# Kernel optimization log

Measured on AMD Instinct MI355X. Metric: run time of the kernel, lower is better.

Reference implementation:

```python
import jax, jax.numpy as jnp
import numpy as np

N = 50000   # nodes
E = 800000  # edges (avg degree 16)
DIMS = [(128, 128), (128, 128), (128, 64)]  # (in, out) per SAGEConv layer
EPS_BN = 1e-5
EPS_NORM = 1e-12


def _make_layer(key, din, dout):
    k1, k2 = jax.random.split(key)
    s = 1.0 / np.sqrt(din)
    return (
        jax.random.normal(k1, (dout, din), jnp.float32) * s,  # Wl: neighbor linear
        jnp.zeros((dout,), jnp.float32),                      # bl
        jax.random.normal(k2, (dout, din), jnp.float32) * s,  # Wr: root linear (no bias in PyG)
        jnp.ones((dout,), jnp.float32),                       # bn gamma
        jnp.zeros((dout,), jnp.float32),                      # bn beta
        jnp.zeros((dout,), jnp.float32),                      # bn running mean
        jnp.ones((dout,), jnp.float32),                       # bn running var
    )


def setup_inputs() -> dict:
    key = jax.random.key(0)
    kx, ke, k0, k1, k2 = jax.random.split(key, 5)
    inp = {
        "x": jax.random.normal(kx, (N, 128), jnp.float32),
        "edge_index": jax.random.randint(ke, (2, E), 0, N, dtype=jnp.int32),
    }
    for i, (k, (din, dout)) in enumerate(zip([k0, k1, k2], DIMS)):
        Wl, bl, Wr, g, b, rm, rv = _make_layer(k, din, dout)
        inp.update({f"Wl{i}": Wl, f"bl{i}": bl, f"Wr{i}": Wr,
                    f"g{i}": g, f"b{i}": b, f"rm{i}": rm, f"rv{i}": rv})
    return inp


def _sage_conv(x, src, dst, Wl, bl, Wr):
    # mean aggregation of incoming messages: gather src features, scatter-add at dst
    agg = jax.ops.segment_sum(x[src], dst, num_segments=N)          # [N, din]
    deg = jax.ops.segment_sum(jnp.ones((src.shape[0],), x.dtype), dst, num_segments=N)
    mean = agg / jnp.maximum(deg, 1.0)[:, None]
    return mean @ Wl.T + bl + x @ Wr.T


def _bn_eval(x, g, b, rm, rv):
    return g * (x - rm) * jax.lax.rsqrt(rv + EPS_BN) + b


def reference(x, edge_index,
              Wl0, bl0, Wr0, g0, b0, rm0, rv0,
              Wl1, bl1, Wr1, g1, b1, rm1, rv1,
              Wl2, bl2, Wr2, g2, b2, rm2, rv2):
    src, dst = edge_index[0], edge_index[1]
    layers = [
        (Wl0, bl0, Wr0, g0, b0, rm0, rv0),
        (Wl1, bl1, Wr1, g1, b1, rm1, rv1),
        (Wl2, bl2, Wr2, g2, b2, rm2, rv2),
    ]
    h = x
    for i, (Wl, bl, Wr, g, b, rm, rv) in enumerate(layers):
        h = _bn_eval(_sage_conv(h, src, dst, Wl, bl, Wr), g, b, rm, rv)
        if i < len(layers) - 1:
            h = jax.nn.relu(h)  # dropout is identity in eval mode
    # F.normalize(p=2, dim=1)
    return h / jnp.maximum(jnp.linalg.norm(h, axis=1, keepdims=True), EPS_NORM)
```

## Files before the change

kernel.cpp:

```cpp
#include <hip/hip_runtime.h>
#include <hip/hip_bf16.h>

#define CDIV(a,b) (((a)+(b)-1)/(b))
#define NBUCK_MAX 512
#define FUSE_CAP 1536
#define CAPL     4096
#define AGGF_CAP 2048

typedef __attribute__((ext_vector_type(8))) short short8;
typedef __attribute__((ext_vector_type(4))) float f32x4;
typedef __attribute__((ext_vector_type(2))) float f32x2;

static __device__ __forceinline__ unsigned short f2bf(float f){
  union { float f; unsigned u; } v; v.f = f;
  unsigned r = v.u + 0x7fffu + ((v.u >> 16) & 1u);
  return (unsigned short)(r >> 16);
}
static __device__ __forceinline__ unsigned pack2(float lo, float hi){
  return (unsigned)f2bf(lo) | ((unsigned)f2bf(hi) << 16);
}
static __device__ __forceinline__ float bf2f(unsigned short s){
  union { unsigned u; float f; } v; v.u = ((unsigned)s) << 16; return v.f;
}
static __device__ __forceinline__ unsigned pk_fp8x4(float a, float b, float c, float d){
// ... 31 lines not shown
      int kc = a.perm ? (((k & 7) << 4) | (k >> 3)) : k;
      v = a.W0[nn*128 + kc];
    } else {
      v = a.W1[nn*128 + (k - 128)];
    }
    a.Bpk[idx] = f2bf(v);
  } else if (a.do_bn && idx < NB16 + a.dout){
    int jj = idx - NB16;
    float s = a.g[jj] * rsqrtf(a.rv[jj] + 1e-5f);
    a.sc[jj] = s;
    a.sh[jj] = (a.bl[jj] - a.rm[jj]) * s + a.b[jj];
  }
}


__global__ __launch_bounds__(256) void k_prep(const float* __restrict__ x, int n4, unsigned* __restrict__ xb,
                                              unsigned* __restrict__ xq,
                                              const int* __restrict__ dst, int E,
                                              int* __restrict__ bcnt, int nbuck,
                                              int castBlocks, int histBlocks,
                                              WtpArgs a0, WtpArgs a1, WtpArgs a2, WtpArgs a3){
  __shared__ int s[NBUCK_MAX];
  int b = blockIdx.x, t = threadIdx.x;
  if (b < castBlocks){
    int i = b*256 + t;
    if (i < n4){
      float4 v = ((const float4*)x)[i];
      uint2 o; o.x = pack2(v.x, v.y); o.y = pack2(v.z, v.w);
      ((uint2*)xb)[i] = o;
      xq[i] = pk_fp8x4(v.x, v.y, v.z, v.w);
    }
    return;
  }
  b -= castBlocks;
  if (b < histBlocks){
    for (int i=t;i<nbuck;i+=256) s[i] = 0;
    __syncthreads();
    constexpr int EPT = 16;
    int e0 = b*256*EPT;
    #pragma unroll
    for (int i=0;i<EPT;i++){
      int e = e0 + i*256 + t;
      if (e < E) atomicAdd(&s[dst[e] >> 7], 1);
    }
    __syncthreads();
    for (int i=t;i<nbuck;i+=256){
      int c = s[i];
      if (c > 0) atomicAdd(&bcnt[i], c);
    }
    return;
  }
  b -= histBlocks;
  if (b < a0.nblk){ wtp_one(a0, b*256 + t); return; }
  b -= a0.nblk;
  if (b < a1.nblk){ wtp_one(a1, b*256 + t); return; }
  b -= a1.nblk;
  if (b < a2.nblk){ wtp_one(a2, b*256 + t); return; }
  b -= a2.nblk;
  wtp_one(a3, b*256 + t);
}

__global__ __launch_bounds__(256) void k_bucketA(const int* __restrict__ src, const int* __restrict__ dst,
                                                 int E, const int* __restrict__ bcnt,
                                                 int* __restrict__ bcur, unsigned* __restrict__ ebuf, int nbuck){
  __shared__ int scnt[NBUCK_MAX];
  __shared__ int sbase[NBUCK_MAX];
  __shared__ int sboff[NBUCK_MAX];
  __shared__ int ss[256];
  int t = threadIdx.x;
  {
    int a0 = (2*t   < nbuck) ? bcnt[2*t]   : 0;
    int a1 = (2*t+1 < nbuck) ? bcnt[2*t+1] : 0;
    ss[t] = a0 + a1; __syncthreads();
    for (int d=1; d<256; d<<=1){
      int u = (t>=d) ? ss[t-d] : 0;
      __syncthreads();
      ss[t] += u;
      __syncthreads();
    }
    int excl = ss[t] - (a0 + a1);
    if (2*t   < nbuck) sboff[2*t]   = excl;
    if (2*t+1 < nbuck) sboff[2*t+1] = excl + a0;
  }
  for (int i=t;i<nbuck;i+=256) scnt[i] = 0;
  __syncthreads();
  constexpr int EPT = 16;
  int e0 = blockIdx.x*256*EPT;
  int b[EPT]; unsigned pk[EPT];
  #pragma unroll
  for (int i=0;i<EPT;i++){
    int e = e0 + i*256 + t;
    if (e < E){
      int d = dst[e];
      b[i] = d >> 7;
      pk[i] = ((unsigned)(d & 127) << 16) | (unsigned)src[e];
      atomicAdd(&scnt[b[i]], 1);
    } else b[i] = -1;
  }
  __syncthreads();
  for (int i=t;i<nbuck;i+=256){
    int c = scnt[i];
    sbase[i] = (c > 0) ? atomicAdd(&bcur[i], c) : 0;
    scnt[i] = 0;
  }
  __syncthreads();
  #pragma unroll
  for (int i=0;i<EPT;i++){
    if (b[i] >= 0){
      int p = atomicAdd(&scnt[b[i]], 1);
      ebuf[(size_t)sboff[b[i]] + sbase[b[i]] + p] = pk[i];
    }
  }
}


__global__ __launch_bounds__(256, 3) void k_bfuse(
    const unsigned* __restrict__ ebuf, const int* __restrict__ bcnt, int nbuck, int E, int N,
    int* __restrict__ off, int* __restrict__ csr,
    const uint4* __restrict__ xq4, const unsigned short* __restrict__ Ag,
    const unsigned short* __restrict__ Bpk, const float* __restrict__ sc, const float* __restrict__ sh,
    unsigned short* __restrict__ outh, unsigned* __restrict__ outq){
  __shared__ uint4 Ms4[64*17];
  __shared__ int scsr[FUSE_CAP];
  __shared__ int sEx[NBUCK_MAX];
  __shared__ int ss[256];
  unsigned short* Ms = (unsigned short*)Ms4;
  int* sdeg = (int*)Ms4;
  int* sabs = sdeg + 128;
  int* cur  = sabs + 129;
  int bb_ = blockIdx.x;
  int b = bb_ >> 1, hi = bb_ & 1;
  int t = threadIdx.x;
  {
    int a0 = (2*t   < nbuck) ? bcnt[2*t]   : 0;
    int a1 = (2*t+1 < nbuck) ? bcnt[2*t+1] : 0;
    ss[t] = a0 + a1; __syncthreads();
    for (int d=1; d<256; d<<=1){
      int u = (t>=d) ? ss[t-d] : 0;
      __syncthreads();
      ss[t] += u;
      __syncthreads();
    }
    int excl = ss[t] - (a0 + a1);
    if (2*t   < nbuck) sEx[2*t]   = excl;
    if (2*t+1 < nbuck) sEx[2*t+1] = excl + a0;
  }
  if (t < 128){ sdeg[t] = 0; cur[t] = 0; }
  __syncthreads();
  int e0 = sEx[b];
  int e1 = (b+1 < nbuck) ? sEx[b+1] : E;
  for (int e = e0 + t; e < e1; e += 256)
    atomicAdd(&sdeg[ebuf[e] >> 16], 1);
  __syncthreads();
  for (int d=1; d<128; d<<=1){
    int u = (t < 128 && t >= d) ? sdeg[t-d] : 0;
    __syncthreads();
    if (t < 128) sdeg[t] += u;
    __syncthreads();
  }
  if (t == 0) sabs[0] = 0;
  if (t < 128) sabs[t+1] = sdeg[t];
  __syncthreads();
  int base64 = sabs[hi*64];
  int myTot  = sabs[hi*64 + 64] - base64;
  int n0 = (b << 7) + hi*64;
  int cnt = (N > n0) ? min(64, N - n0) : 0;
  if (cnt > 0 && t <= cnt) off[n0 + t] = e0 + sabs[hi*64 + t];
  int lane = t & 63, w = t >> 6, sl = lane & 7;
  int gs0[2], gs1[2];
  #pragma unroll
  for (int it=0; it<2; it++){
    int rk = w*16 + it*8 + (lane >> 3);
    gs0[it] = sabs[hi*64 + rk] - base64;
    gs1[it] = sabs[hi*64 + rk + 1] - base64;
  }
  bool fits = myTot <= FUSE_CAP;
  for (int e = e0 + t; e < e1; e += 256){
    unsigned pr = ebuf[e];
    int ln = (int)(pr >> 16);
    if ((ln >> 6) == hi){
      int p = atomicAdd(&cur[ln], 1);
      int gpos = sabs[ln] + p;
      int sv = (int)(pr & 0xffffu);
      if (fits) scsr[gpos - base64] = sv;
      else      csr[e0 + gpos] = sv;
    }
  }
  __syncthreads();
  const int* gcsr = csr + e0 + base64;
  if (fits){
    for (int i = t; i < myTot; i += 256) csr[e0 + base64 + i] = scsr[i];
  } else {
    for (int i = t; i < FUSE_CAP; i += 256) scsr[i] = gcsr[i];
    __syncthreads();
  }

  #pragma unroll
  for (int it=0; it<2; it++){
    int rk = w*16 + it*8 + (lane >> 3);
    int s0 = gs0[it], s1 = gs1[it];
    f32x2 b0={0,0},b1={0,0},b2={0,0},b3={0,0},b4={0,0},b5={0,0},b6={0,0},b7={0,0};
    int e = s0;
    for (; e + 8 <= s1; e += 8){
      int i0,i1,i2,i3,i4,i5,i6,i7;
      if (e + 8 <= FUSE_CAP){
        i0 = scsr[e];   i1 = scsr[e+1]; i2 = scsr[e+2]; i3 = scsr[e+3];
        i4 = scsr[e+4]; i5 = scsr[e+5]; i6 = scsr[e+6]; i7 = scsr[e+7];
      } else {
        i0 = gcsr[e];   i1 = gcsr[e+1]; i2 = gcsr[e+2]; i3 = gcsr[e+3];
        i4 = gcsr[e+4]; i5 = gcsr[e+5]; i6 = gcsr[e+6]; i7 = gcsr[e+7];
      }
// ... 29 lines not shown
    int d = s1 - s0;
    float inv = 1.0f / (float)(d > 0 ? d : 1);
    uint4 o0, o1;
    o0.x = pack2(b0.x*inv, b0.y*inv);  o0.y = pack2(b1.x*inv, b1.y*inv);
    o0.z = pack2(b2.x*inv, b2.y*inv);  o0.w = pack2(b3.x*inv, b3.y*inv);
    o1.x = pack2(b4.x*inv, b4.y*inv);  o1.y = pack2(b5.x*inv, b5.y*inv);
    o1.z = pack2(b6.x*inv, b6.y*inv);  o1.w = pack2(b7.x*inv, b7.y*inv);
    Ms4[rk*17 + sl*2]     = o0;
    Ms4[rk*17 + sl*2 + 1] = o1;
  }
  __syncthreads();

  int quad = lane >> 4, c = lane & 15;
  int woff = w*16;
  int r0 = n0 + woff + c;

  f32x4 acc[8];
  #pragma unroll
  for (int nt=0;nt<8;nt++) acc[nt] = (f32x4){0.f,0.f,0.f,0.f};

  #pragma unroll
  for (int kk=0; kk<8; kk++){
    int ka = (kk & 3)*32 + quad*8;
    short8 a0;
    if (kk < 4){
      a0 = *(const short8*)&Ms[(woff + c)*136 + ka];
    } else {
      a0 = (short8){0,0,0,0,0,0,0,0};
      if (r0 < N) a0 = *(const short8*)(Ag + (size_t)r0*128 + ka);
    }
    #pragma unroll
    for (int nt=0; nt<8; nt++){
      short8 bb2 = *(const short8*)(Bpk + (size_t)((kk*8 + nt)*64 + lane)*8);
      acc[nt] = __builtin_amdgcn_mfma_f32_16x16x32_bf16(a0, bb2, acc[nt], 0, 0, 0);
    }
  }

  float scv[8], shv[8];
  #pragma unroll
  for (int nt=0;nt<8;nt++){ scv[nt] = sc[nt*16 + c]; shv[nt] = sh[nt*16 + c]; }

  #pragma unroll
  for (int r=0;r<4;r++){
    int row = n0 + woff + quad*4 + r;
    if (row < N){
      float u[8];
      #pragma unroll
      for (int nt=0;nt<8;nt++){
        float uu = acc[nt][r]*scv[nt] + shv[nt];
        u[nt] = fmaxf(uu, 0.f);
        outh[(size_t)row*128 + nt*16 + c] = f2bf(u[nt]);
      }
      uint2 q;
      q.x = pk_fp8x4(u[0], u[1], u[2], u[3]);
      q.y = pk_fp8x4(u[4], u[5], u[6], u[7]);
      ((uint2*)outq)[(size_t)row*16 + c] = q;
    }
  }
}


__global__ __launch_bounds__(256, 3) void k_fuse1(
    const uint4* __restrict__ hq4, const int* __restrict__ off, const int* __restrict__ csr,
    const unsigned short* __restrict__ Ag, const unsigned short* __restrict__ Bpk,
    const float* __restrict__ sc, const float* __restrict__ sh,
    const unsigned short* __restrict__ BpkL,
    unsigned short* __restrict__ outh, unsigned* __restrict__ outyl, int n){
  __shared__ uint4 Ms4[64*17];
  __shared__ uint4 sBL4[1024];
  __shared__ int sw[2];
  unsigned short* Ms = (unsigned short*)Ms4;
  int* scsr = (int*)sBL4;
  int t = threadIdx.x;
  int n0 = blockIdx.x*64;
  if (t < 2) sw[t] = off[min(n0 + t*64, n)];
  __syncthreads();
  int e0b = sw[0];
  int span = sw[1] - e0b;
  for (int i = t; i < span && i < CAPL; i += 256) scsr[i] = csr[e0b + i];
  __syncthreads();

  int lane = t & 63, w = t >> 6;
  int sl = lane & 7;

  #pragma unroll
  for (int it=0; it<2; it++){
    int rk = w*16 + it*8 + (lane >> 3);
    int idx = n0 + rk;
    bool valid = idx < n;
    int s0 = valid ? off[idx]   : 0;
    int s1 = valid ? off[idx+1] : 0;
    f32x2 b0={0,0},b1={0,0},b2={0,0},b3={0,0},b4={0,0},b5={0,0},b6={0,0},b7={0,0};
    int e = s0;
    for (; e + 8 <= s1; e += 8){
      int le = e - e0b;
      int i0,i1,i2,i3,i4,i5,i6,i7;
      if (le + 8 <= CAPL){
        i0 = scsr[le];   i1 = scsr[le+1]; i2 = scsr[le+2]; i3 = scsr[le+3];
        i4 = scsr[le+4]; i5 = scsr[le+5]; i6 = scsr[le+6]; i7 = scsr[le+7];
      } else {
        i0 = csr[e];   i1 = csr[e+1]; i2 = csr[e+2]; i3 = csr[e+3];
        i4 = csr[e+4]; i5 = csr[e+5]; i6 = csr[e+6]; i7 = csr[e+7];
      }
      uint4 v0 = hq4[(size_t)i0*8 + sl];
      uint4 v1 = hq4[(size_t)i1*8 + sl];
      uint4 v2 = hq4[(size_t)i2*8 + sl];
      uint4 v3 = hq4[(size_t)i3*8 + sl];
      uint4 v4 = hq4[(size_t)i4*8 + sl];
      uint4 v5 = hq4[(size_t)i5*8 + sl];
      uint4 v6 = hq4[(size_t)i6*8 + sl];
      uint4 v7 = hq4[(size_t)i7*8 + sl];
      ACCP16(v0); ACCP16(v1); ACCP16(v2); ACCP16(v3);
      ACCP16(v4); ACCP16(v5); ACCP16(v6); ACCP16(v7);
    }
    for (; e + 4 <= s1; e += 4){
      int le = e - e0b;
      int i0,i1,i2,i3;
      if (le + 4 <= CAPL){
        i0 = scsr[le]; i1 = scsr[le+1]; i2 = scsr[le+2]; i3 = scsr[le+3];
      } else {
        i0 = csr[e]; i1 = csr[e+1]; i2 = csr[e+2]; i3 = csr[e+3];
      }
      uint4 v0 = hq4[(size_t)i0*8 + sl];
      uint4 v1 = hq4[(size_t)i1*8 + sl];
      uint4 v2 = hq4[(size_t)i2*8 + sl];
      uint4 v3 = hq4[(size_t)i3*8 + sl];
      ACCP16(v0); ACCP16(v1); ACCP16(v2); ACCP16(v3);
    }
    for (; e < s1; e++){
      int le = e - e0b;
      int ii = (le < CAPL) ? scsr[le] : csr[e];
      uint4 v = hq4[(size_t)ii*8 + sl];
      ACCP16(v);
    }
    int d = s1 - s0;
    float inv = 1.0f / (float)(d > 0 ? d : 1);
    uint4 o0, o1;
    o0.x = pack2(b0.x*inv, b0.y*inv);  o0.y = pack2(b1.x*inv, b1.y*inv);
    o0.z = pack2(b2.x*inv, b2.y*inv);  o0.w = pack2(b3.x*inv, b3.y*inv);
    o1.x = pack2(b4.x*inv, b4.y*inv);  o1.y = pack2(b5.x*inv, b5.y*inv);
    o1.z = pack2(b6.x*inv, b6.y*inv);  o1.w = pack2(b7.x*inv, b7.y*inv);
    Ms4[rk*17 + sl*2]     = o0;
    Ms4[rk*17 + sl*2 + 1] = o1;
  }
  __syncthreads();

  int quad = lane >> 4, c = lane & 15;
  int woff = w*16;
  int r0 = n0 + woff + c;

  f32x4 acc[8];
  #pragma unroll
  for (int nt=0;nt<8;nt++) acc[nt] = (f32x4){0.f,0.f,0.f,0.f};

  #pragma unroll
  for (int kk=0; kk<8; kk++){
    int ka = (kk & 3)*32 + quad*8;
    short8 a0;
    if (kk < 4){
      a0 = *(const short8*)&Ms[(woff + c)*136 + ka];
    } else {
      a0 = (short8){0,0,0,0,0,0,0,0};
      if (r0 < n) a0 = *(const short8*)(Ag + (size_t)r0*128 + ka);
    }
    #pragma unroll
    for (int nt=0; nt<8; nt++){
      short8 bb2 = *(const short8*)(Bpk + (size_t)((kk*8 + nt)*64 + lane)*8);
      acc[nt] = __builtin_amdgcn_mfma_f32_16x16x32_bf16(a0, bb2, acc[nt], 0, 0, 0);
    }
  }

  float scv[8], shv[8];
  #pragma unroll
  for (int nt=0;nt<8;nt++){ scv[nt] = sc[nt*16 + c]; shv[nt] = sh[nt*16 + c]; }

  __syncthreads();

  #pragma unroll
  for (int r=0;r<4;r++){
    int lrow = woff + quad*4 + r;
    int row = n0 + lrow;
    if (row < n){
      float u[8];
      #pragma unroll
      for (int nt=0;nt<8;nt++){
        float uu = acc[nt][r]*scv[nt] + shv[nt];
        u[nt] = fmaxf(uu, 0.f);
        outh[(size_t)row*128 + nt*16 + c] = f2bf(u[nt]);
      }
      #pragma unroll
      for (int nt=0;nt<8;nt++) Ms[lrow*136 + nt*16 + c] = f2bf(u[nt]);
    } else {
      #pragma unroll
      for (int nt=0;nt<8;nt++) Ms[lrow*136 + nt*16 + c] = 0;
    }
  }

  {
    const uint4* sL = (const uint4*)BpkL;
    #pragma unroll
    for (int i=0;i<4;i++) sBL4[i*256 + t] = sL[i*256 + t];
  }
  __syncthreads();
  unsigned short* BsL = (unsigned short*)sBL4;
  f32x4 acc2[4];
  #pragma unroll
  for (int nt=0;nt<4;nt++) acc2[nt] = (f32x4){0.f,0.f,0.f,0.f};
  int r0l = woff + c;
  #pragma unroll
  for (int kk=0; kk<4; kk++){
    int ka = kk*32 + quad*8;
    short8 a0 = *(const short8*)&Ms[r0l*136 + ka];
    #pragma unroll
    for (int nt=0; nt<4; nt++){
      short8 bb2 = *(const short8*)&BsL[(size_t)((kk*4 + nt)*64 + lane)*8];
      acc2[nt] = __builtin_amdgcn_mfma_f32_16x16x32_bf16(a0, bb2, acc2[nt], 0, 0, 0);
    }
  }
  #pragma unroll
  for (int r=0;r<4;r++){
    int row = n0 + woff + quad*4 + r;
    if (row < n){
      unsigned q = pk_fp8x4(acc2[0][r], acc2[1][r], acc2[2][r], acc2[3][r]);
      outyl[(size_t)row*16 + c] = q;
    }
  }
}


__global__ __launch_bounds__(256, 3) void k_aggf(
    const uint4* __restrict__ ylq4, const int* __restrict__ off, const int* __restrict__ csr,
    const unsigned short* __restrict__ A0, const unsigned short* __restrict__ BpkR,
    const float* __restrict__ sc, const float* __restrict__ sh,
    float* __restrict__ outf, int n){
  __shared__ unsigned short Ms[64*64];
  __shared__ unsigned short Bs[128*64];
  __shared__ int scsr[AGGF_CAP];
  __shared__ int sw[2];
  int t = threadIdx.x;
  int n0 = blockIdx.x*64;
  if (t < 2) sw[t] = off[min(n0 + t*64, n)];
  {
    const uint4* s = (const uint4*)BpkR;
    uint4* d = (uint4*)Bs;
    #pragma unroll
    for (int i=0;i<4;i++) d[i*256 + t] = s[i*256 + t];
  }
  __syncthreads();
  int e0b = sw[0];
  int span = sw[1] - e0b;
  for (int i = t; i < span && i < AGGF_CAP; i += 256) scsr[i] = csr[e0b + i];
  __syncthreads();

  int lane = t & 63, w = t >> 6;
  int sl4 = lane & 3;

  {
    int rk = w*16 + (lane >> 2);
    int idx = n0 + rk;
    bool valid = idx < n;
    int s0 = valid ? off[idx]   : 0;
    int s1 = valid ? off[idx+1] : 0;
    f32x2 b0={0,0},b1={0,0},b2={0,0},b3={0,0},b4={0,0},b5={0,0},b6={0,0},b7={0,0};
    int e = s0;
    for (; e + 8 <= s1; e += 8){
      int le = e - e0b;
      int i0,i1,i2,i3,i4,i5,i6,i7;
      if (le + 8 <= AGGF_CAP){
        i0 = scsr[le];   i1 = scsr[le+1]; i2 = scsr[le+2]; i3 = scsr[le+3];
        i4 = scsr[le+4]; i5 = scsr[le+5]; i6 = scsr[le+6]; i7 = scsr[le+7];
      } else {
        i0 = csr[e];   i1 = csr[e+1]; i2 = csr[e+2]; i3 = csr[e+3];
        i4 = csr[e+4]; i5 = csr[e+5]; i6 = csr[e+6]; i7 = csr[e+7];
      }
      uint4 v0 = ylq4[(size_t)i0*4 + sl4];
      uint4 v1 = ylq4[(size_t)i1*4 + sl4];
      uint4 v2 = ylq4[(size_t)i2*4 + sl4];
      uint4 v3 = ylq4[(size_t)i3*4 + sl4];
      uint4 v4 = ylq4[(size_t)i4*4 + sl4];
      uint4 v5 = ylq4[(size_t)i5*4 + sl4];
      uint4 v6 = ylq4[(size_t)i6*4 + sl4];
      uint4 v7 = ylq4[(size_t)i7*4 + sl4];
      ACCP16(v0); ACCP16(v1); ACCP16(v2); ACCP16(v3);
      ACCP16(v4); ACCP16(v5); ACCP16(v6); ACCP16(v7);
    }
    for (; e + 4 <= s1; e += 4){
      int le = e - e0b;
      int i0,i1,i2,i3;
      if (le + 4 <= AGGF_CAP){
        i0 = scsr[le]; i1 = scsr[le+1]; i2 = scsr[le+2]; i3 = scsr[le+3];
      } else {
        i0 = csr[e]; i1 = csr[e+1]; i2 = csr[e+2]; i3 = csr[e+3];
      }
      uint4 v0 = ylq4[(size_t)i0*4 + sl4];
      uint4 v1 = ylq4[(size_t)i1*4 + sl4];
      uint4 v2 = ylq4[(size_t)i2*4 + sl4];
      uint4 v3 = ylq4[(size_t)i3*4 + sl4];
      ACCP16(v0); ACCP16(v1); ACCP16(v2); ACCP16(v3);
    }
    for (; e < s1; e++){
      int le = e - e0b;
      int ii = (le < AGGF_CAP) ? scsr[le] : csr[e];
      uint4 v = ylq4[(size_t)ii*4 + sl4];
      ACCP16(v);
    }
    int d = s1 - s0;
    float inv = 1.0f / (float)(d > 0 ? d : 1);
    uint4 o0, o1;
    o0.x = pack2(b0.x*inv, b0.y*inv);  o0.y = pack2(b1.x*inv, b1.y*inv);
    o0.z = pack2(b2.x*inv, b2.y*inv);  o0.w = pack2(b3.x*inv, b3.y*inv);
    o1.x = pack2(b4.x*inv, b4.y*inv);  o1.y = pack2(b5.x*inv, b5.y*inv);
    o1.z = pack2(b6.x*inv, b6.y*inv);  o1.w = pack2(b7.x*inv, b7.y*inv);
    ((uint4*)Ms)[rk*8 + sl4*2]     = o0;
    ((uint4*)Ms)[rk*8 + sl4*2 + 1] = o1;
  }
  __syncthreads();

  int quad = lane >> 4, c = lane & 15;
  int woff = w*16;
  int r0 = n0 + woff + c;
  f32x4 acc[4];
  #pragma unroll
  for (int nt=0;nt<4;nt++) acc[nt] = (f32x4){0.f,0.f,0.f,0.f};
  #pragma unroll
  for (int kk=0; kk<4; kk++){
    int ka = kk*32 + quad*8;
    short8 a0 = {0,0,0,0,0,0,0,0};
    if (r0 < n) a0 = *(const short8*)(A0 + (size_t)r0*128 + ka);
    #pragma unroll
    for (int nt=0; nt<4; nt++){
      short8 bb2 = *(const short8*)&Bs[(size_t)((kk*4 + nt)*64 + lane)*8];
      acc[nt] = __builtin_amdgcn_mfma_f32_16x16x32_bf16(a0, bb2, acc[nt], 0, 0, 0);
    }
  }

  float scv[4], shv[4];
  #pragma unroll
  for (int nt=0;nt<4;nt++){ scv[nt] = sc[nt*16 + c]; shv[nt] = sh[nt*16 + c]; }

  #pragma unroll
  for (int r=0;r<4;r++){
    int lr = woff + quad*4 + r;
    int row = n0 + lr;
    float v[4];
    float ss2 = 0.f;
    if (row < n){
      #pragma unroll
      for (int nt=0;nt<4;nt++){
        float u = acc[nt][r] + bf2f(Ms[lr*64 + c*4 + nt]);
        u = u*scv[nt] + shv[nt];
        v[nt] = u;
        ss2 += u*u;
      }
    } else {
      #pragma unroll
      for (int nt=0;nt<4;nt++) v[nt] = 0.f;
    }
    ss2 += __shfl_xor(ss2, 1, 64);
    ss2 += __shfl_xor(ss2, 2, 64);
    ss2 += __shfl_xor(ss2, 4, 64);
    ss2 += __shfl_xor(ss2, 8, 64);
    float rn = 1.0f / fmaxf(sqrtf(ss2), 1e-12f);
    if (row < n){
      #pragma unroll
      for (int nt=0;nt<4;nt++) outf[(size_t)row*64 + nt*16 + c] = v[nt]*rn;
    }
  }
}


extern "C" void kernel_launch(void* const* d_in, const int* in_sizes, int n_in,
                              void* d_out, int out_size, void* d_ws, size_t ws_size,
                              hipStream_t stream){
  const float* x = (const float*)d_in[0];
  const int* ei  = (const int*)d_in[1];
  int N = in_sizes[0] / 128;
  int E = in_sizes[1] / 2;
  const int* esrc = ei;
  const int* edst = ei + E;
  int nbuck = CDIV(N, 128);
  int nb2 = 2*nbuck;

  const float *Wl[3], *bl[3], *Wr[3], *g[3], *bb[3], *rm[3], *rv[3];
  int dout[3];
  for (int i=0;i<3;i++){
    int base = 2 + 7*i;
    Wl[i]=(const float*)d_in[base];   bl[i]=(const float*)d_in[base+1];
    Wr[i]=(const float*)d_in[base+2]; g[i] =(const float*)d_in[base+3];
    bb[i]=(const float*)d_in[base+4]; rm[i]=(const float*)d_in[base+5];
    rv[i]=(const float*)d_in[base+6];
    dout[i] = in_sizes[base] / 128;
  }

  char* p = (char*)d_ws;
  size_t o = 0;
  auto alloc = [&](size_t bytes)->void*{ void* r = p + o; o += (bytes + 255) & ~(size_t)255; return r; };
  int* bz    = (int*)alloc((size_t)2*nbuck*4);
  int* bcnt  = bz;
  int* bcur  = bz + nbuck;
  int* off   = (int*)alloc((size_t)(N+1)*4);
  int* csr   = (int*)alloc((size_t)E*4);
  unsigned* ebuf = (unsigned*)alloc((size_t)E*4);
  unsigned* xb   = (unsigned*)alloc((size_t)N*64*4);
  unsigned* xq   = (unsigned*)alloc((size_t)N*128);
  unsigned* h_a  = (unsigned*)alloc((size_t)N*64*4);
  unsigned* haq  = (unsigned*)alloc((size_t)N*128);
  unsigned* h_b  = (unsigned*)alloc((size_t)N*64*4);
  unsigned* ylb  = (unsigned*)alloc((size_t)N*64);
  unsigned short* Bpk01[2];
  float* sc[3]; float* sh[3];
  for (int i=0;i<2;i++) Bpk01[i] = (unsigned short*)alloc((size_t)256*dout[i]*2);
  unsigned short* BpkL = (unsigned short*)alloc((size_t)128*dout[2]*2);
  unsigned short* BpkR = (unsigned short*)alloc((size_t)128*dout[2]*2);
  for (int i=0;i<3;i++){
    sc[i] = (float*)alloc((size_t)dout[i]*4);
    sh[i] = (float*)alloc((size_t)dout[i]*4);
  }

  hipMemsetAsync(bz, 0, (size_t)2*nbuck*4, stream);

  WtpArgs wa[4];
  wa[0] = { Wl[0], Wr[0], bl[0], g[0], bb[0], rm[0], rv[0], Bpk01[0], sc[0], sh[0], 8, dout[0], 1, CDIV(256*dout[0]+dout[0],256), 0 };
  wa[1] = { Wl[1], Wr[1], bl[1], g[1], bb[1], rm[1], rv[1], Bpk01[1], sc[1], sh[1], 8, dout[1], 1, CDIV(256*dout[1]+dout[1],256), 1 };
  wa[2] = { Wl[2], nullptr, nullptr, nullptr, nullptr, nullptr, nullptr, BpkL, nullptr, nullptr, 4, dout[2], 0, CDIV(128*dout[2],256), 0 };
  wa[3] = { Wr[2], nullptr, bl[2], g[2], bb[2], rm[2], rv[2], BpkR, sc[2], sh[2], 4, dout[2], 1, CDIV(128*dout[2]+dout[2],256), 0 };

  int castBlocks = CDIV(N*32, 256);
  int histBlocks = CDIV(E, 256*16);
  int prepBlocks = castBlocks + histBlocks + wa[0].nblk + wa[1].nblk + wa[2].nblk + wa[3].nblk;
  k_prep   <<<prepBlocks,256,0,stream>>>(x, N*32, xb, xq, edst, E, bcnt, nbuck, castBlocks, histBlocks,
                                         wa[0], wa[1], wa[2], wa[3]);
  k_bucketA<<<CDIV(E,256*16),256,0,stream>>>(esrc, edst, E, bcnt, bcur, ebuf, nbuck);

  k_bfuse<<<nb2,256,0,stream>>>(ebuf, bcnt, nbuck, E, N, off, csr,
                                (const uint4*)xq, (const unsigned short*)xb,
                                Bpk01[0], sc[0], sh[0],
                                (unsigned short*)h_a, haq);
  k_fuse1<<<nb2,256,0,stream>>>((const uint4*)haq, off, csr,
                                (const unsigned short*)h_a, Bpk01[1], sc[1], sh[1], BpkL,
                                (unsigned short*)h_b, ylb, N);
  k_aggf<<<nb2,256,0,stream>>>((const uint4*)ylb, off, csr,
                               (const unsigned short*)h_b, BpkR, sc[2], sh[2],
                               (float*)d_out, N);
}
```

Measured before the change: 226.0 us.

## Merge five pipeline kernels into one persistent kernel with grid barriers

Replaces the five separate launches (prep, bucket, bfuse, fuse1, aggf) with a single persistent kernel sized to occupancy. The phases are separated by a software global barrier built on atomic counters, and each phase's work blocks run through grid-stride loops over a shared LDS pool. The bucket phase also halves its edges per block. This is meant to remove launch gaps and tail idle time between kernels. In exchange it adds barrier spin cost, caps occupancy at 2 blocks per CU, and depends on every block being co-resident.

After: 659.2 us. +191.7%, slower.

```diff
diff --git a/kernel.cpp b/kernel.cpp
--- a/kernel.cpp
+++ b/kernel.cpp
@@ -69,63 +69,96 @@
 }
 
 
-__global__ __launch_bounds__(256) void k_prep(const float* __restrict__ x, int n4, unsigned* __restrict__ xb,
-                                              unsigned* __restrict__ xq,
-                                              const int* __restrict__ dst, int E,
-                                              int* __restrict__ bcnt, int nbuck,
-                                              int castBlocks, int histBlocks,
-                                              WtpArgs a0, WtpArgs a1, WtpArgs a2, WtpArgs a3){
-  __shared__ int s[NBUCK_MAX];
-  int b = blockIdx.x, t = threadIdx.x;
-  if (b < castBlocks){
+struct MegaArgs {
+  const float* x; int n4;
+  unsigned* xb; unsigned* xq;
+  const int* esrc; const int* edst;
+  int E, N, nbuck;
+  int* bcnt; int* bcur;
+  int* barCnt; int* barEpoch;
+  int* off; int* csr; unsigned* ebuf;
+  const unsigned short* Bpk0; const unsigned short* Bpk1;
+  const unsigned short* BpkL; const unsigned short* BpkR;
+  const float *sc0, *sh0, *sc1, *sh1, *sc2, *sh2;
+  unsigned short* h_a; unsigned short* h_b;
+  unsigned* haq; unsigned* ylb;
+  float* outf;
+  int castBlocks, histBlocks, p0Total, aBlocks, nb2, nblk;
+  WtpArgs wa0, wa1, wa2, wa3;
+};
+
+static __device__ __forceinline__ void gbar(int* cnt, int* epoch, int nblk, int eps){
+  __syncthreads();
+  if (threadIdx.x == 0){
+    __threadfence();
+    int prev = __hip_atomic_fetch_add(cnt, 1, __ATOMIC_ACQ_REL, __HIP_MEMORY_SCOPE_AGENT);
+    if (prev == nblk - 1){
+      __hip_atomic_store(cnt, 0, __ATOMIC_RELAXED, __HIP_MEMORY_SCOPE_AGENT);
+      __hip_atomic_fetch_add(epoch, 1, __ATOMIC_RELEASE, __HIP_MEMORY_SCOPE_AGENT);
+    } else {
+      while (__hip_atomic_load(epoch, __ATOMIC_ACQUIRE, __HIP_MEMORY_SCOPE_AGENT) < eps){
+        __builtin_amdgcn_s_sleep(2);
+      }
+    }
+  }
+  __syncthreads();
+  __threadfence();
+}
+
+
+static __device__ void p0_prep(int b, uint4* pool4, const MegaArgs& A){
+  int* s = (int*)pool4;
+  int t = threadIdx.x;
+  __syncthreads();
+  if (b < A.castBlocks){
     int i = b*256 + t;
-    if (i < n4){
-      float4 v = ((const float4*)x)[i];
+    if (i < A.n4){
+      float4 v = ((const float4*)A.x)[i];
       uint2 o; o.x = pack2(v.x, v.y); o.y = pack2(v.z, v.w);
-      ((uint2*)xb)[i] = o;
-      xq[i] = pk_fp8x4(v.x, v.y, v.z, v.w);
+      ((uint2*)A.xb)[i] = o;
+      A.xq[i] = pk_fp8x4(v.x, v.y, v.z, v.w);
     }
     return;
   }
-  b -= castBlocks;
-  if (b < histBlocks){
-    for (int i=t;i<nbuck;i+=256) s[i] = 0;
+  b -= A.castBlocks;
+  if (b < A.histBlocks){
+    for (int i=t;i<A.nbuck;i+=256) s[i] = 0;
     __syncthreads();
     constexpr int EPT = 16;
     int e0 = b*256*EPT;
     #pragma unroll
     for (int i=0;i<EPT;i++){
       int e = e0 + i*256 + t;
-      if (e < E) atomicAdd(&s[dst[e] >> 7], 1);
+      if (e < A.E) atomicAdd(&s[A.edst[e] >> 7], 1);
     }
     __syncthreads();
-    for (int i=t;i<nbuck;i+=256){
+    for (int i=t;i<A.nbuck;i+=256){
       int c = s[i];
-      if (c > 0) atomicAdd(&bcnt[i], c);
+      if (c > 0) atomicAdd(&A.bcnt[i], c);
     }
     return;
   }
-  b -= histBlocks;
-  if (b < a0.nblk){ wtp_one(a0, b*256 + t); return; }
-  b -= a0.nblk;
-  if (b < a1.nblk){ wtp_one(a1, b*256 + t); return; }
-  b -= a1.nblk;
-  if (b < a2.nblk){ wtp_one(a2, b*256 + t); return; }
-  b -= a2.nblk;
-  wtp_one(a3, b*256 + t);
-}
-
-__global__ __launch_bounds__(256) void k_bucketA(const int* __restrict__ src, const int* __restrict__ dst,
-                                                 int E, const int* __restrict__ bcnt,
-                                                 int* __restrict__ bcur, unsigned* __restrict__ ebuf, int nbuck){
-  __shared__ int scnt[NBUCK_MAX];
-  __shared__ int sbase[NBUCK_MAX];
-  __shared__ int sboff[NBUCK_MAX];
-  __shared__ int ss[256];
+  b -= A.histBlocks;
+  if (b < A.wa0.nblk){ wtp_one(A.wa0, b*256 + t); return; }
+  b -= A.wa0.nblk;
+  if (b < A.wa1.nblk){ wtp_one(A.wa1, b*256 + t); return; }
+  b -= A.wa1.nblk;
+  if (b < A.wa2.nblk){ wtp_one(A.wa2, b*256 + t); return; }
+  b -= A.wa2.nblk;
+  wtp_one(A.wa3, b*256 + t);
+}
+
+
+static __device__ void p1_bucketA(int blk, uint4* pool4, const MegaArgs& A){
+  int* scnt  = (int*)pool4;
+  int* sbase = scnt + NBUCK_MAX;
+  int* sboff = sbase + NBUCK_MAX;
+  int* ss    = sboff + NBUCK_MAX;
   int t = threadIdx.x;
+  __syncthreads();
   {
-    int a0 = (2*t   < nbuck) ? bcnt[2*t]   : 0;
-    int a1 = (2*t+1 < nbuck) ? bcnt[2*t+1] : 0;
+    int a0 = (2*t   < A.nbuck) ? A.bcnt[2*t]   : 0;
+    int a1 = (2*t+1 < A.nbuck) ? A.bcnt[2*t+1] : 0;
     ss[t] = a0 + a1; __syncthreads();
     for (int d=1; d<256; d<<=1){
       int u = (t>=d) ? ss[t-d] : 0;
@@ -134,61 +167,56 @@
       __syncthreads();
     }
     int excl = ss[t] - (a0 + a1);
-    if (2*t   < nbuck) sboff[2*t]   = excl;
-    if (2*t+1 < nbuck) sboff[2*t+1] = excl + a0;
-  }
-  for (int i=t;i<nbuck;i+=256) scnt[i] = 0;
-  __syncthreads();
-  constexpr int EPT = 16;
-  int e0 = blockIdx.x*256*EPT;
-  int b[EPT]; unsigned pk[EPT];
+    if (2*t   < A.nbuck) sboff[2*t]   = excl;
+    if (2*t+1 < A.nbuck) sboff[2*t+1] = excl + a0;
+  }
+  for (int i=t;i<A.nbuck;i+=256) scnt[i] = 0;
+  __syncthreads();
+  constexpr int EPT = 8;
+  int e0 = blk*256*EPT;
+  int bb[EPT]; unsigned pk[EPT];
   #pragma unroll
   for (int i=0;i<EPT;i++){
     int e = e0 + i*256 + t;
-    if (e < E){
-      int d = dst[e];
-      b[i] = d >> 7;
-      pk[i] = ((unsigned)(d & 127) << 16) | (unsigned)src[e];
-      atomicAdd(&scnt[b[i]], 1);
-    } else b[i] = -1;
-  }
-  __syncthreads();
-  for (int i=t;i<nbuck;i+=256){
+    if (e < A.E){
+      int d = A.edst[e];
+      bb[i] = d >> 7;
+      pk[i] = ((unsigned)(d & 127) << 16) | (unsigned)A.esrc[e];
+      atomicAdd(&scnt[bb[i]], 1);
+    } else bb[i] = -1;
+  }
+  __syncthreads();
+  for (int i=t;i<A.nbuck;i+=256){
     int c = scnt[i];
-    sbase[i] = (c > 0) ? atomicAdd(&bcur[i], c) : 0;
+    sbase[i] = (c > 0) ? atomicAdd(&A.bcur[i], c) : 0;
     scnt[i] = 0;
   }
   __syncthreads();
   #pragma unroll
   for (int i=0;i<EPT;i++){
-    if (b[i] >= 0){
-      int p = atomicAdd(&scnt[b[i]], 1);
-      ebuf[(size_t)sboff[b[i]] + sbase[b[i]] + p] = pk[i];
-    }
-  }
-}
-
-
-__global__ __launch_bounds__(256, 3) void k_bfuse(
-    const unsigned* __restrict__ ebuf, const int* __restrict__ bcnt, int nbuck, int E, int N,
-    int* __restrict__ off, int* __restrict__ csr,
-    const uint4* __restrict__ xq4, const unsigned short* __restrict__ Ag,
-    const unsigned short* __restrict__ Bpk, const float* __restrict__ sc, const float* __restrict__ sh,
-    unsigned short* __restrict__ outh, unsigned* __restrict__ outq){
-  __shared__ uint4 Ms4[64*17];
-  __shared__ int scsr[FUSE_CAP];
-  __shared__ int sEx[NBUCK_MAX];
-  __shared__ int ss[256];
+    if (bb[i] >= 0){
+      int p = atomicAdd(&scnt[bb[i]], 1);
+      A.ebuf[(size_t)sboff[bb[i]] + sbase[bb[i]] + p] = pk[i];
+    }
+  }
+}
+
+
+static __device__ void p2_bfuse(int wb, uint4* pool4, const MegaArgs& A){
+  uint4* Ms4 = pool4;
+  int* scsr  = (int*)(pool4 + 1088);
+  int* sEx   = (int*)(pool4 + 1472);
+  int* ss    = (int*)(pool4 + 1600);
   unsigned short* Ms = (unsigned short*)Ms4;
   int* sdeg = (int*)Ms4;
   int* sabs = sdeg + 128;
   int* cur  = sabs + 129;
-  int bb_ = blockIdx.x;
-  int b = bb_ >> 1, hi = bb_ & 1;
+  int b = wb >> 1, hi = wb & 1;
   int t = threadIdx.x;
+  __syncthreads();
   {
-    int a0 = (2*t   < nbuck) ? bcnt[2*t]   : 0;
-    int a1 = (2*t+1 < nbuck) ? bcnt[2*t+1] : 0;
+    int a0 = (2*t   < A.nbuck) ? A.bcnt[2*t]   : 0;
+    int a1 = (2*t+1 < A.nbuck) ? A.bcnt[2*t+1] : 0;
     ss[t] = a0 + a1; __syncthreads();
     for (int d=1; d<256; d<<=1){
       int u = (t>=d) ? ss[t-d] : 0;
@@ -197,15 +225,15 @@
       __syncthreads();
     }
     int excl = ss[t] - (a0 + a1);
-    if (2*t   < nbuck) sEx[2*t]   = excl;
-    if (2*t+1 < nbuck) sEx[2*t+1] = excl + a0;
+    if (2*t   < A.nbuck) sEx[2*t]   = excl;
+    if (2*t+1 < A.nbuck) sEx[2*t+1] = excl + a0;
   }
   if (t < 128){ sdeg[t] = 0; cur[t] = 0; }
   __syncthreads();
   int e0 = sEx[b];
-  int e1 = (b+1 < nbuck) ? sEx[b+1] : E;
+  int e1 = (b+1 < A.nbuck) ? sEx[b+1] : A.E;
   for (int e = e0 + t; e < e1; e += 256)
-    atomicAdd(&sdeg[ebuf[e] >> 16], 1);
+    atomicAdd(&sdeg[A.ebuf[e] >> 16], 1);
   __syncthreads();
   for (int d=1; d<128; d<<=1){
     int u = (t < 128 && t >= d) ? sdeg[t-d] : 0;
@@ -219,8 +247,8 @@
   int base64 = sabs[hi*64];
   int myTot  = sabs[hi*64 + 64] - base64;
   int n0 = (b << 7) + hi*64;
-  int cnt = (N > n0) ? min(64, N - n0) : 0;
-  if (cnt > 0 && t <= cnt) off[n0 + t] = e0 + sabs[hi*64 + t];
+  int cnt = (A.N > n0) ? min(64, A.N - n0) : 0;
+  if (cnt > 0 && t <= cnt) A.off[n0 + t] = e0 + sabs[hi*64 + t];
   int lane = t & 63, w = t >> 6, sl = lane & 7;
   int gs0[2], gs1[2];
   #pragma unroll
@@ -231,25 +259,26 @@
   }
   bool fits = myTot <= FUSE_CAP;
   for (int e = e0 + t; e < e1; e += 256){
-    unsigned pr = ebuf[e];
+    unsigned pr = A.ebuf[e];
     int ln = (int)(pr >> 16);
     if ((ln >> 6) == hi){
       int p = atomicAdd(&cur[ln], 1);
       int gpos = sabs[ln] + p;
       int sv = (int)(pr & 0xffffu);
       if (fits) scsr[gpos - base64] = sv;
-      else      csr[e0 + gpos] = sv;
-    }
-  }
-  __syncthreads();
-  const int* gcsr = csr + e0 + base64;
+      else      A.csr[e0 + gpos] = sv;
+    }
+  }
+  __syncthreads();
+  const int* gcsr = A.csr + e0 + base64;
   if (fits){
-    for (int i = t; i < myTot; i += 256) csr[e0 + base64 + i] = scsr[i];
+    for (int i = t; i < myTot; i += 256) A.csr[e0 + base64 + i] = scsr[i];
   } else {
     for (int i = t; i < FUSE_CAP; i += 256) scsr[i] = gcsr[i];
     __syncthreads();
   }
 
+  const uint4* xq4 = (const uint4*)A.xq;
   #pragma unroll
   for (int it=0; it<2; it++){
     int rk = w*16 + it*8 + (lane >> 3);
@@ -309,11 +338,10 @@
   int quad = lane >> 4, c = lane & 15;
   int woff = w*16;
   int r0 = n0 + woff + c;
-
+  const unsigned short* Ag = (const unsigned short*)A.xb;
   f32x4 acc[8];
   #pragma unroll
   for (int nt=0;nt<8;nt++) acc[nt] = (f32x4){0.f,0.f,0.f,0.f};
-
   #pragma unroll
   for (int kk=0; kk<8; kk++){
     int ka = (kk & 3)*32 + quad*8;
@@ -322,69 +350,64 @@
       a0 = *(const short8*)&Ms[(woff + c)*136 + ka];
     } else {
       a0 = (short8){0,0,0,0,0,0,0,0};
-      if (r0 < N) a0 = *(const short8*)(Ag + (size_t)r0*128 + ka);
+      if (r0 < A.N) a0 = *(const short8*)(Ag + (size_t)r0*128 + ka);
     }
     #pragma unroll
     for (int nt=0; nt<8; nt++){
-      short8 bb2 = *(const short8*)(Bpk + (size_t)((kk*8 + nt)*64 + lane)*8);
+      short8 bb2 = *(const short8*)(A.Bpk0 + (size_t)((kk*8 + nt)*64 + lane)*8);
       acc[nt] = __builtin_amdgcn_mfma_f32_16x16x32_bf16(a0, bb2, acc[nt], 0, 0, 0);
     }
   }
-
   float scv[8], shv[8];
   #pragma unroll
-  for (int nt=0;nt<8;nt++){ scv[nt] = sc[nt*16 + c]; shv[nt] = sh[nt*16 + c]; }
-
+  for (int nt=0;nt<8;nt++){ scv[nt] = A.sc0[nt*16 + c]; shv[nt] = A.sh0[nt*16 + c]; }
   #pragma unroll
   for (int r=0;r<4;r++){
     int row = n0 + woff + quad*4 + r;
-    if (row < N){
+    if (row < A.N){
       float u[8];
       #pragma unroll
       for (int nt=0;nt<8;nt++){
         float uu = acc[nt][r]*scv[nt] + shv[nt];
         u[nt] = fmaxf(uu, 0.f);
-        outh[(size_t)row*128 + nt*16 + c] = f2bf(u[nt]);
+        A.h_a[(size_t)row*128 + nt*16 + c] = f2bf(u[nt]);
       }
       uint2 q;
       q.x = pk_fp8x4(u[0], u[1], u[2], u[3]);
       q.y = pk_fp8x4(u[4], u[5], u[6], u[7]);
-      ((uint2*)outq)[(size_t)row*16 + c] = q;
-    }
-  }
-}
-
-
-__global__ __launch_bounds__(256, 3) void k_fuse1(
-    const uint4* __restrict__ hq4, const int* __restrict__ off, const int* __restrict__ csr,
-    const unsigned short* __restrict__ Ag, const unsigned short* __restrict__ Bpk,
-    const float* __restrict__ sc, const float* __restrict__ sh,
-    const unsigned short* __restrict__ BpkL,
-    unsigned short* __restrict__ outh, unsigned* __restrict__ outyl, int n){
-  __shared__ uint4 Ms4[64*17];
-  __shared__ uint4 sBL4[1024];
-  __shared__ int sw[2];
+      ((uint2*)A.haq)[(size_t)row*16 + c] = q;
+    }
+  }
+}
+
+
+static __device__ void p3_fuse1(int wb, uint4* pool4, const MegaArgs& A){
+  uint4* Ms4  = pool4;
+  uint4* sBL4 = pool4 + 1088;
+  int* sw     = (int*)(pool4 + 2112);
   unsigned short* Ms = (unsigned short*)Ms4;
   int* scsr = (int*)sBL4;
   int t = threadIdx.x;
-  int n0 = blockIdx.x*64;
-  if (t < 2) sw[t] = off[min(n0 + t*64, n)];
+  __syncthreads();
+  int n0 = wb*64;
+  if (t < 2) sw[t] = A.off[min(n0 + t*64, A.N)];
   __syncthreads();
   int e0b = sw[0];
   int span = sw[1] - e0b;
-  for (int i = t; i < span && i < CAPL; i += 256) scsr[i] = csr[e0b + i];
+  for (int i = t; i < span && i < CAPL; i += 256) scsr[i] = A.csr[e0b + i];
   __syncthreads();
 
   int lane = t & 63, w = t >> 6;
   int sl = lane & 7;
+  const uint4* hq4 = (const uint4*)A.haq;
 
   #pragma unroll
   for (int it=0; it<2; it++){
     int rk = w*16 + it*8 + (lane >> 3);
     int idx = n0 + rk;
-    bool valid = idx < n;
-    int s0 = valid ? off[idx]   : 0;
-    int s1 = valid ? off[idx+1] : 0;
+    bool valid = idx < A.N;
+    int s0 = valid ? A.off[idx]   : 0;
+    int s1 = valid ? A.off[idx+1] : 0;
     f32x2 b0={0,0},b1={0,0},b2={0,0},b3={0,0},b4={0,0},b5={0,0},b6={0,0},b7={0,0};
     int e = s0;
     for (; e + 8 <= s1; e += 8){
@@ -394,8 +417,8 @@
         i0 = scsr[le];   i1 = scsr[le+1]; i2 = scsr[le+2]; i3 = scsr[le+3];
         i4 = scsr[le+4]; i5 = scsr[le+5]; i6 = scsr[le+6]; i7 = scsr[le+7];
       } else {
-        i0 = csr[e];   i1 = csr[e+1]; i2 = csr[e+2]; i3 = csr[e+3];
-        i4 = csr[e+4]; i5 = csr[e+5]; i6 = csr[e+6]; i7 = csr[e+7];
+        i0 = A.csr[e];   i1 = A.csr[e+1]; i2 = A.csr[e+2]; i3 = A.csr[e+3];
+        i4 = A.csr[e+4]; i5 = A.csr[e+5]; i6 = A.csr[e+6]; i7 = A.csr[e+7];
       }
       uint4 v0 = hq4[(size_t)i0*8 + sl];
       uint4 v1 = hq4[(size_t)i1*8 + sl];
@@ -414,7 +437,7 @@
       if (le + 4 <= CAPL){
         i0 = scsr[le]; i1 = scsr[le+1]; i2 = scsr[le+2]; i3 = scsr[le+3];
       } else {
-        i0 = csr[e]; i1 = csr[e+1]; i2 = csr[e+2]; i3 = csr[e+3];
+        i0 = A.csr[e]; i1 = A.csr[e+1]; i2 = A.csr[e+2]; i3 = A.csr[e+3];
       }
       uint4 v0 = hq4[(size_t)i0*8 + sl];
       uint4 v1 = hq4[(size_t)i1*8 + sl];
@@ -424,7 +447,7 @@
     }
     for (; e < s1; e++){
       int le = e - e0b;
-      int ii = (le < CAPL) ? scsr[le] : csr[e];
+      int ii = (le < CAPL) ? scsr[le] : A.csr[e];
       uint4 v = hq4[(size_t)ii*8 + sl];
       ACCP16(v);
     }
@@ -443,11 +466,9 @@
   int quad = lane >> 4, c = lane & 15;
   int woff = w*16;
   int r0 = n0 + woff + c;
-
   f32x4 acc[8];
   #pragma unroll
   for (int nt=0;nt<8;nt++) acc[nt] = (f32x4){0.f,0.f,0.f,0.f};
-
   #pragma unroll
   for (int kk=0; kk<8; kk++){
     int ka = (kk & 3)*32 + quad*8;
@@ -456,32 +477,29 @@
       a0 = *(const short8*)&Ms[(woff + c)*136 + ka];
     } else {
       a0 = (short8){0,0,0,0,0,0,0,0};
-      if (r0 < n) a0 = *(const short8*)(Ag + (size_t)r0*128 + ka);
+      if (r0 < A.N) a0 = *(const short8*)(A.h_a + (size_t)r0*128 + ka);
     }
     #pragma unroll
     for (int nt=0; nt<8; nt++){
-      short8 bb2 = *(const short8*)(Bpk + (size_t)((kk*8 + nt)*64 + lane)*8);
+      short8 bb2 = *(const short8*)(A.Bpk1 + (size_t)((kk*8 + nt)*64 + lane)*8);
       acc[nt] = __builtin_amdgcn_mfma_f32_16x16x32_bf16(a0, bb2, acc[nt], 0, 0, 0);
     }
   }
-
   float scv[8], shv[8];
   #pragma unroll
-  for (int nt=0;nt<8;nt++){ scv[nt] = sc[nt*16 + c]; shv[nt] = sh[nt*16 + c]; }
-
-  __syncthreads();
-
+  for (int nt=0;nt<8;nt++){ scv[nt] = A.sc1[nt*16 + c]; shv[nt] = A.sh1[nt*16 + c]; }
+  __syncthreads();
   #pragma unroll
   for (int r=0;r<4;r++){
     int lrow = woff + quad*4 + r;
     int row = n0 + lrow;
-    if (row < n){
+    if (row < A.N){
       float u[8];
       #pragma unroll
       for (int nt=0;nt<8;nt++){
         float uu = acc[nt][r]*scv[nt] + shv[nt];
         u[nt] = fmaxf(uu, 0.f);
-        outh[(size_t)row*128 + nt*16 + c] = f2bf(u[nt]);
+        A.h_b[(size_t)row*128 + nt*16 + c] = f2bf(u[nt]);
       }
       #pragma unroll
       for (int nt=0;nt<8;nt++) Ms[lrow*136 + nt*16 + c] = f2bf(u[nt]);
@@ -490,9 +508,8 @@
       for (int nt=0;nt<8;nt++) Ms[lrow*136 + nt*16 + c] = 0;
     }
   }
-
   {
-    const uint4* sL = (const uint4*)BpkL;
+    const uint4* sL = (const uint4*)A.BpkL;
     #pragma unroll
     for (int i=0;i<4;i++) sBL4[i*256 + t] = sL[i*256 + t];
   }
@@ -515,28 +532,25 @@
   #pragma unroll
   for (int r=0;r<4;r++){
     int row = n0 + woff + quad*4 + r;
-    if (row < n){
+    if (row < A.N){
       unsigned q = pk_fp8x4(acc2[0][r], acc2[1][r], acc2[2][r], acc2[3][r]);
-      outyl[(size_t)row*16 + c] = q;
-    }
-  }
-}
-
-
-__global__ __launch_bounds__(256, 3) void k_aggf(
-    const uint4* __restrict__ ylq4, const int* __restrict__ off, const int* __restrict__ csr,
-    const unsigned short* __restrict__ A0, const unsigned short* __restrict__ BpkR,
-    const float* __restrict__ sc, const float* __restrict__ sh,
-    float* __restrict__ outf, int n){
-  __shared__ unsigned short Ms[64*64];
-  __shared__ unsigned short Bs[128*64];
-  __shared__ int scsr[AGGF_CAP];
-  __shared__ int sw[2];
+      A.ylb[(size_t)row*16 + c] = q;
+    }
+  }
+}
+
+
+static __device__ void p4_aggf(int wb, uint4* pool4, const MegaArgs& A){
+  unsigned short* Ms = (unsigned short*)pool4;
+  unsigned short* Bs = (unsigned short*)(pool4 + 512);
+  int* scsr = (int*)(pool4 + 1536);
+  int* sw   = (int*)(pool4 + 2048);
   int t = threadIdx.x;
-  int n0 = blockIdx.x*64;
-  if (t < 2) sw[t] = off[min(n0 + t*64, n)];
+  __syncthreads();
+  int n0 = wb*64;
+  if (t < 2) sw[t] = A.off[min(n0 + t*64, A.N)];
   {
-    const uint4* s = (const uint4*)BpkR;
+    const uint4* s = (const uint4*)A.BpkR;
     uint4* d = (uint4*)Bs;
     #pragma unroll
     for (int i=0;i<4;i++) d[i*256 + t] = s[i*256 + t];
@@ -544,18 +558,19 @@
   __syncthreads();
   int e0b = sw[0];
   int span = sw[1] - e0b;
-  for (int i = t; i < span && i < AGGF_CAP; i += 256) scsr[i] = csr[e0b + i];
+  for (int i = t; i < span && i < AGGF_CAP; i += 256) scsr[i] = A.csr[e0b + i];
   __syncthreads();
 
   int lane = t & 63, w = t >> 6;
   int sl4 = lane & 3;
+  const uint4* ylq4 = (const uint4*)A.ylb;
 
   {
     int rk = w*16 + (lane >> 2);
     int idx = n0 + rk;
-    bool valid = idx < n;
-    int s0 = valid ? off[idx]   : 0;
-    int s1 = valid ? off[idx+1] : 0;
+    bool valid = idx < A.N;
+    int s0 = valid ? A.off[idx]   : 0;
+    int s1 = valid ? A.off[idx+1] : 0;
     f32x2 b0={0,0},b1={0,0},b2={0,0},b3={0,0},b4={0,0},b5={0,0},b6={0,0},b7={0,0};
     int e = s0;
     for (; e + 8 <= s1; e += 8){
@@ -565,8 +580,8 @@
         i0 = scsr[le];   i1 = scsr[le+1]; i2 = scsr[le+2]; i3 = scsr[le+3];
         i4 = scsr[le+4]; i5 = scsr[le+5]; i6 = scsr[le+6]; i7 = scsr[le+7];
       } else {
-        i0 = csr[e];   i1 = csr[e+1]; i2 = csr[e+2]; i3 = csr[e+3];
-        i4 = csr[e+4]; i5 = csr[e+5]; i6 = csr[e+6]; i7 = csr[e+7];
+        i0 = A.csr[e];   i1 = A.csr[e+1]; i2 = A.csr[e+2]; i3 = A.csr[e+3];
+        i4 = A.csr[e+4]; i5 = A.csr[e+5]; i6 = A.csr[e+6]; i7 = A.csr[e+7];
       }
       uint4 v0 = ylq4[(size_t)i0*4 + sl4];
       uint4 v1 = ylq4[(size_t)i1*4 + sl4];
@@ -585,7 +600,7 @@
       if (le + 4 <= AGGF_CAP){
         i0 = scsr[le]; i1 = scsr[le+1]; i2 = scsr[le+2]; i3 = scsr[le+3];
       } else {
-        i0 = csr[e]; i1 = csr[e+1]; i2 = csr[e+2]; i3 = csr[e+3];
+        i0 = A.csr[e]; i1 = A.csr[e+1]; i2 = A.csr[e+2]; i3 = A.csr[e+3];
       }
       uint4 v0 = ylq4[(size_t)i0*4 + sl4];
       uint4 v1 = ylq4[(size_t)i1*4 + sl4];
@@ -595,7 +610,7 @@
     }
     for (; e < s1; e++){
       int le = e - e0b;
-      int ii = (le < AGGF_CAP) ? scsr[le] : csr[e];
+      int ii = (le < AGGF_CAP) ? scsr[le] : A.csr[e];
       uint4 v = ylq4[(size_t)ii*4 + sl4];
       ACCP16(v);
     }
@@ -621,25 +636,23 @@
   for (int kk=0; kk<4; kk++){
     int ka = kk*32 + quad*8;
     short8 a0 = {0,0,0,0,0,0,0,0};
-    if (r0 < n) a0 = *(const short8*)(A0 + (size_t)r0*128 + ka);
+    if (r0 < A.N) a0 = *(const short8*)(A.h_b + (size_t)r0*128 + ka);
     #pragma unroll
     for (int nt=0; nt<4; nt++){
       short8 bb2 = *(const short8*)&Bs[(size_t)((kk*4 + nt)*64 + lane)*8];
       acc[nt] = __builtin_amdgcn_mfma_f32_16x16x32_bf16(a0, bb2, acc[nt], 0, 0, 0);
     }
   }
-
   float scv[4], shv[4];
   #pragma unroll
-  for (int nt=0;nt<4;nt++){ scv[nt] = sc[nt*16 + c]; shv[nt] = sh[nt*16 + c]; }
-
+  for (int nt=0;nt<4;nt++){ scv[nt] = A.sc2[nt*16 + c]; shv[nt] = A.sh2[nt*16 + c]; }
   #pragma unroll
   for (int r=0;r<4;r++){
     int lr = woff + quad*4 + r;
     int row = n0 + lr;
     float v[4];
     float ss2 = 0.f;
-    if (row < n){
+    if (row < A.N){
       #pragma unroll
       for (int nt=0;nt<4;nt++){
         float u = acc[nt][r] + bf2f(Ms[lr*64 + c*4 + nt]);
@@ -656,11 +669,25 @@
     ss2 += __shfl_xor(ss2, 4, 64);
     ss2 += __shfl_xor(ss2, 8, 64);
     float rn = 1.0f / fmaxf(sqrtf(ss2), 1e-12f);
-    if (row < n){
+    if (row < A.N){
       #pragma unroll
-      for (int nt=0;nt<4;nt++) outf[(size_t)row*64 + nt*16 + c] = v[nt]*rn;
-    }
-  }
+      for (int nt=0;nt<4;nt++) A.outf[(size_t)row*64 + nt*16 + c] = v[nt]*rn;
+    }
+  }
+}
+
+
+__global__ __launch_bounds__(256, 2) void k_mega(MegaArgs A){
+  __shared__ uint4 pool4[2120];
+  for (int wb = blockIdx.x; wb < A.p0Total; wb += gridDim.x) p0_prep(wb, pool4, A);
+  gbar(A.barCnt, A.barEpoch, A.nblk, 1);
+  for (int wb = blockIdx.x; wb < A.aBlocks; wb += gridDim.x) p1_bucketA(wb, pool4, A);
+  gbar(A.barCnt, A.barEpoch, A.nblk, 2);
+  for (int wb = blockIdx.x; wb < A.nb2; wb += gridDim.x) p2_bfuse(wb, pool4, A);
+  gbar(A.barCnt, A.barEpoch, A.nblk, 3);
+  for (int wb = blockIdx.x; wb < A.nb2; wb += gridDim.x) p3_fuse1(wb, pool4, A);
+  gbar(A.barCnt, A.barEpoch, A.nblk, 4);
+  for (int wb = blockIdx.x; wb < A.nb2; wb += gridDim.x) p4_aggf(wb, pool4, A);
 }
 
 
@@ -690,9 +717,11 @@
   char* p = (char*)d_ws;
   size_t o = 0;
   auto alloc = [&](size_t bytes)->void*{ void* r = p + o; o += (bytes + 255) & ~(size_t)255; return r; };
-  int* bz    = (int*)alloc((size_t)2*nbuck*4);
+  int* bz    = (int*)alloc((size_t)(2*nbuck + 2)*4);
   int* bcnt  = bz;
   int* bcur  = bz + nbuck;
+  int* barCnt   = bz + 2*nbuck;
+  int* barEpoch = bz + 2*nbuck + 1;
   int* off   = (int*)alloc((size_t)(N+1)*4);
   int* csr   = (int*)alloc((size_t)E*4);
   unsigned* ebuf = (unsigned*)alloc((size_t)E*4);
@@ -712,29 +741,39 @@
     sh[i] = (float*)alloc((size_t)dout[i]*4);
   }
 
-  hipMemsetAsync(bz, 0, (size_t)2*nbuck*4, stream);
-
-  WtpArgs wa[4];
-  wa[0] = { Wl[0], Wr[0], bl[0], g[0], bb[0], rm[0], rv[0], Bpk01[0], sc[0], sh[0], 8, dout[0], 1, CDIV(256*dout[0]+dout[0],256), 0 };
-  wa[1] = { Wl[1], Wr[1], bl[1], g[1], bb[1], rm[1], rv[1], Bpk01[1], sc[1], sh[1], 8, dout[1], 1, CDIV(256*dout[1]+dout[1],256), 1 };
-  wa[2] = { Wl[2], nullptr, nullptr, nullptr, nullptr, nullptr, nullptr, BpkL, nullptr, nullptr, 4, dout[2], 0, CDIV(128*dout[2],256), 0 };
-  wa[3] = { Wr[2], nullptr, bl[2], g[2], bb[2], rm[2], rv[2], BpkR, sc[2], sh[2], 4, dout[2], 1, CDIV(128*dout[2]+dout[2],256), 0 };
-
-  int castBlocks = CDIV(N*32, 256);
-  int histBlocks = CDIV(E, 256*16);
-  int prepBlocks = castBlocks + histBlocks + wa[0].nblk + wa[1].nblk + wa[2].nblk + wa[3].nblk;
-  k_prep   <<<prepBlocks,256,0,stream>>>(x, N*32, xb, xq, edst, E, bcnt, nbuck, castBlocks, histBlocks,
-                                         wa[0], wa[1], wa[2], wa[3]);
-  k_bucketA<<<CDIV(E,256*16),256,0,stream>>>(esrc, edst, E, bcnt, bcur, ebuf, nbuck);
-
-  k_bfuse<<<nb2,256,0,stream>>>(ebuf, bcnt, nbuck, E, N, off, csr,
-                                (const uint4*)xq, (const unsigned short*)xb,
-                                Bpk01[0], sc[0], sh[0],
-                                (unsigned short*)h_a, haq);
-  k_fuse1<<<nb2,256,0,stream>>>((const uint4*)haq, off, csr,
-                                (const unsigned short*)h_a, Bpk01[1], sc[1], sh[1], BpkL,
-                                (unsigned short*)h_b, ylb, N);
-  k_aggf<<<nb2,256,0,stream>>>((const uint4*)ylb, off, csr,
-                               (const unsigned short*)h_b, BpkR, sc[2], sh[2],
-                               (float*)d_out, N);
-}
+  hipMemsetAsync(bz, 0, (size_t)(2*nbuck + 2)*4, stream);
+
+  MegaArgs ma;
+  ma.x = x; ma.n4 = N*32;
+  ma.xb = xb; ma.xq = xq;
+  ma.esrc = esrc; ma.edst = edst;
+  ma.E = E; ma.N = N; ma.nbuck = nbuck;
+  ma.bcnt = bcnt; ma.bcur = bcur;
+  ma.barCnt = barCnt; ma.barEpoch = barEpoch;
+  ma.off = off; ma.csr = csr; ma.ebuf = ebuf;
+  ma.Bpk0 = Bpk01[0]; ma.Bpk1 = Bpk01[1]; ma.BpkL = BpkL; ma.BpkR = BpkR;
+  ma.sc0 = sc[0]; ma.sh0 = sh[0]; ma.sc1 = sc[1]; ma.sh1 = sh[1]; ma.sc2 = sc[2]; ma.sh2 = sh[2];
+  ma.h_a = (unsigned short*)h_a; ma.h_b = (unsigned short*)h_b;
+  ma.haq = haq; ma.ylb = ylb;
+  ma.outf = (float*)d_out;
+  ma.wa0 = { Wl[0], Wr[0], bl[0], g[0], bb[0], rm[0], rv[0], Bpk01[0], sc[0], sh[0], 8, dout[0], 1, CDIV(256*dout[0]+dout[0],256), 0 };
+  ma.wa1 = { Wl[1], Wr[1], bl[1], g[1], bb[1], rm[1], rv[1], Bpk01[1], sc[1], sh[1], 8, dout[1], 1, CDIV(256*dout[1]+dout[1],256), 1 };
+  ma.wa2 = { Wl[2], nullptr, nullptr, nullptr, nullptr, nullptr, nullptr, BpkL, nullptr, nullptr, 4, dout[2], 0, CDIV(128*dout[2],256), 0 };
+  ma.wa3 = { Wr[2], nullptr, bl[2], g[2], bb[2], rm[2], rv[2], BpkR, sc[2], sh[2], 4, dout[2], 1, CDIV(128*dout[2]+dout[2],256), 0 };
+  ma.castBlocks = CDIV(N*32, 256);
+  ma.histBlocks = CDIV(E, 256*16);
+  ma.p0Total = ma.castBlocks + ma.histBlocks + ma.wa0.nblk + ma.wa1.nblk + ma.wa2.nblk + ma.wa3.nblk;
+  ma.aBlocks = CDIV(E, 256*8);
+  ma.nb2 = nb2;
+
+  static int g_grid = 0;
+  if (g_grid == 0){
+    int perCU = 0, cus = 0;
+    if (hipOccupancyMaxActiveBlocksPerMultiprocessor(&perCU, k_mega, 256, 0) != hipSuccess || perCU < 1) perCU = 2;
+    if (hipDeviceGetAttribute(&cus, hipDeviceAttributeMultiprocessorCount, 0) != hipSuccess || cus < 1) cus = 256;
+    g_grid = perCU * cus;
+  }
+  ma.nblk = g_grid;
+
+  k_mega<<<g_grid, 256, 0, stream>>>(ma);
+}
```
